# Kernel optimization log

Measured on AMD Instinct MI355X. Metric: run time of the kernel, lower is better.

## Reference

```python
import jax, jax.numpy as jnp
import numpy as np

N_MELS = 128
N_STATE = 1024
N_HEAD = 8
N_LAYER = 6
STRIDE = 2
HEAD_DIM = N_STATE // N_HEAD  # 128; must equal N_MELS for the rope buffer to broadcast
B = 8
T = 4096


def setup_inputs():
    key = jax.random.key(0)
    ks = iter(jax.random.split(key, 40))
    def rn(shape, s=0.02):
        return jax.random.normal(next(ks), shape, dtype=jnp.float32) * s
    L, D, F = N_LAYER, N_STATE, 4 * N_STATE
    inp = {}
    inp['x'] = jax.random.normal(next(ks), (B, N_MELS, T), dtype=jnp.float32)
    inp['x_len'] = jax.random.randint(next(ks), (B,), T // 2, T + 1)
    inp['conv1_w'] = rn((D, N_MELS, 3))
    inp['conv1_b'] = jnp.zeros((D,), jnp.float32)
    inp['conv2_w'] = rn((D, D, 3))
    inp['conv2_b'] = jnp.zeros((D,), jnp.float32)
    inp['attn_ln_w'] = jnp.ones((L, D), jnp.float32)
    inp['attn_ln_b'] = jnp.zeros((L, D), jnp.float32)
    inp['q_w'] = rn((L, D, D)); inp['q_b'] = jnp.zeros((L, D), jnp.float32)
    inp['k_w'] = rn((L, D, D))
    inp['v_w'] = rn((L, D, D)); inp['v_b'] = jnp.zeros((L, D), jnp.float32)
    inp['out_w'] = rn((L, D, D)); inp['out_b'] = jnp.zeros((L, D), jnp.float32)
    inp['mlp_ln_w'] = jnp.ones((L, D), jnp.float32)
    inp['mlp_ln_b'] = jnp.zeros((L, D), jnp.float32)
    inp['mlp1_w'] = rn((L, F, D)); inp['mlp1_b'] = jnp.zeros((L, F), jnp.float32)
    inp['mlp2_w'] = rn((L, D, F)); inp['mlp2_b'] = jnp.zeros((L, D), jnp.float32)
    return inp


def _ln(x, w, b, eps=1e-5):
    x = x.astype(jnp.float32)
    m = jnp.mean(x, -1, keepdims=True)
    v = jnp.mean((x - m) ** 2, -1, keepdims=True)
    return (x - m) * jax.lax.rsqrt(v + eps) * w + b


def _conv1d(x, w, b, stride):
    # x: [B, Cin, T]; w: [Cout, Cin, K] (torch OIH layout); pad=1
    y = jax.lax.conv_general_dilated(x, w, (stride,), [(1, 1)],
                                     dimension_numbers=('NCH', 'OIH', 'NCH'))
    return y + b[None, :, None]


def reference(x, x_len, conv1_w, conv1_b, conv2_w, conv2_b,
              attn_ln_w, attn_ln_b, q_w, q_b, k_w, v_w, v_b, out_w, out_b,
              mlp_ln_w, mlp_ln_b, mlp1_w, mlp1_b, mlp2_w, mlp2_b):
    Tin = x.shape[-1]
    h = jax.nn.gelu(_conv1d(x, conv1_w, conv1_b, STRIDE), approximate=False)
    h = jax.nn.gelu(_conv1d(h, conv2_w, conv2_b, 2), approximate=False)
    h = jnp.transpose(h, (0, 2, 1))  # [B, S, D]
    S = h.shape[1]

    # non-pad mask over original mel frames, subsampled like the conv stack
    mask = jnp.arange(Tin)[None, :] < x_len[:, None]
    mask = mask[:, (Tin + 1) % 2::2]
    if STRIDE == 2:
        Tm = mask.shape[-1]
        mask = mask[:, (Tm + 1) % 2::2]
    bias = ((1.0 - mask.astype(jnp.float32)) * -1.0e10)[:, None, None, :]  # [B,1,1,S]

    # rotary embedding table (freqs_cis as cos/sin), dim == HEAD_DIM == N_MELS
    half = HEAD_DIM // 2
    freqs = 1.0 / (10000.0 ** (jnp.arange(0, HEAD_DIM, 2, dtype=jnp.float32) / HEAD_DIM))
    ang = jnp.arange(S, dtype=jnp.float32)[:, None] * freqs[None, :]  # [S, half]
    cos = jnp.cos(ang)[None, :, None, :]
    sin = jnp.sin(ang)[None, :, None, :]
    scale = HEAD_DIM ** (-0.25)

    def rot(t):  # t: [B,S,H,HEAD_DIM], interleaved (re, im) pairs
        tr = t.reshape(t.shape[0], t.shape[1], N_HEAD, half, 2)
        re, im = tr[..., 0], tr[..., 1]
        return jnp.stack([re * cos - im * sin, re * sin + im * cos], -1)\
                  .reshape(t.shape[0], t.shape[1], N_HEAD, HEAD_DIM)

    def block(carry, p):
        aw, ab, qw, qb, kw, vw, vb, ow, ob, mw, mb, w1, b1, w2, b2 = p
        y = _ln(carry, aw, ab)
        q = y @ qw.T + qb
        k = y @ kw.T          # key has no bias
        v = y @ vw.T + vb
        Bb, Ss = q.shape[0], q.shape[1]
        q = rot(q.reshape(Bb, Ss, N_HEAD, HEAD_DIM)) * scale
        k = rot(k.reshape(Bb, Ss, N_HEAD, HEAD_DIM)) * scale
        v = v.reshape(Bb, Ss, N_HEAD, HEAD_DIM)
        qk = jnp.einsum('bqhd,bkhd->bhqk', q, k) + bias
        w = jax.nn.softmax(qk.astype(jnp.float32), axis=-1)
        o = jnp.einsum('bhqk,bkhd->bqhd', w, v).reshape(Bb, Ss, N_STATE)
        carry = carry + o @ ow.T + ob
        y = _ln(carry, mw, mb)
        y = jax.nn.gelu(y @ w1.T + b1, approximate=False) @ w2.T + b2
        return carry + y, None

    params = (attn_ln_w, attn_ln_b, q_w, q_b, k_w, v_w, v_b, out_w, out_b,
              mlp_ln_w, mlp_ln_b, mlp1_w, mlp1_b, mlp2_w, mlp2_b)
    h, _ = jax.lax.scan(block, h, params)

    y_len = (x_len + 1) // 2
    if STRIDE == 2:
        y_len = (y_len + 1) // 2
    return h, y_len
```

## Files before the change

kernel.cpp:

```cpp
#include <hip/hip_runtime.h>
#include <hip/hip_bf16.h>
#include <cstdint>
#include <cstddef>


typedef __bf16 bf16_t;
typedef __bf16 bf16x8 __attribute__((ext_vector_type(8)));
typedef __bf16 bf16x4 __attribute__((ext_vector_type(4)));
typedef float  floatx4 __attribute__((ext_vector_type(4)));

#define NB   8
#define NS   1024
#define ND   1024
#define NT   4096
#define NT1  2048

#define MFMA16(a, b, c) __builtin_amdgcn_mfma_f32_16x16x32_bf16(a, b, c, 0, 0, 0)

#define SBAR() do { __builtin_amdgcn_sched_barrier(0); \
                    __builtin_amdgcn_s_barrier();      \
                    __builtin_amdgcn_sched_barrier(0); } while (0)

__device__ __forceinline__ float gelu_f(float x) {
  const float t = 1.5957691216057308f * (x + 0.044715f * x * x * x);
  return x / (1.0f + __expf(-t));
}

__device__ __forceinline__ void gload16(const void* g, void* l) {
  __builtin_amdgcn_global_load_lds(
      (__attribute__((address_space(1))) void*)(const_cast<void*>(g)),
      (__attribute__((address_space(3))) void*)l, 16, 0, 0);
}

enum { EPI_BF16 = 0, EPI_GELU_BF16 = 2, EPI_GELU_F32 = 3, EPI_RES_F32 = 4, EPI_QKV = 5 };

template<int EPI>
__global__ __launch_bounds__(512)
void gemm_bt(const bf16_t* __restrict__ A, long lda,
             const bf16_t* __restrict__ Bm, long ldb,
             void* Cv, long ldc,
             const float* __restrict__ bias, const float* res,
             int K, int swz,
             bf16_t* out2, bf16_t* out3, const float* __restrict__ bias2,
             const float2* __restrict__ rtab)
{
  __shared__ bf16_t sA[3][4096];
  __shared__ bf16_t sB[3][4096];
  const int tid  = threadIdx.x;
  const int wid  = tid >> 6;
  const int lane = tid & 63;
  const int lo = lane & 15, g = lane >> 4;
  const int wr = wid >> 2, wc = wid & 3;

  int bx = blockIdx.x, by = blockIdx.y;
  if (swz) {
    const int gx = gridDim.x;
    const int n  = gx * gridDim.y;
    int id = bx + by * gx;
    id = (id & 7) * (n >> 3) + (id >> 3);
    bx = id % gx; by = id / gx;
  }
  const int m0 = bx * 128, n0 = by * 128;
  const int NTK = K >> 5;

  const int lrow = lane >> 2;
  const int lcol = 8 * ((lane & 3) ^ ((lane >> 3) & 3));

  auto stage = [&](int t) {
    if (t >= NTK) return;
    const int kb = t << 5;
    bf16_t* dA = &sA[t % 3][0];
    bf16_t* dB = &sB[t % 3][0];
    const int seg = wid;
    gload16(A  + (long)(m0 + seg * 16 + lrow) * lda + kb + lcol, dA + seg * 512);
    gload16(Bm + (long)(n0 + seg * 16 + lrow) * ldb + kb + lcol, dB + seg * 512);
  };

  const int rslot = 16 * (g ^ ((lo >> 1) & 3));

  floatx4 acc[4][2] = {};

  stage(0); stage(1);
  asm volatile("s_waitcnt vmcnt(2)" ::: "memory");
  SBAR();

#pragma unroll 1
  for (int s = 0; s < NTK; ++s) {
    stage(s + 2);
    const bf16_t* bufA = &sA[s % 3][0];
    const bf16_t* bufB = &sB[s % 3][0];
    bf16x8 av[4], bv[2];
#pragma unroll
    for (int i = 0; i < 4; ++i)
      av[i] = *(const bf16x8*)((const char*)(bufA + (wr * 64 + i * 16 + lo) * 32) + rslot);
#pragma unroll
    for (int i = 0; i < 2; ++i)
      bv[i] = *(const bf16x8*)((const char*)(bufB + (wc * 32 + i * 16 + lo) * 32) + rslot);
#pragma unroll
    for (int mi = 0; mi < 4; ++mi)
#pragma unroll
      for (int ni = 0; ni < 2; ++ni)
        acc[mi][ni] = MFMA16(av[mi], bv[ni], acc[mi][ni]);
    if (s + 2 < NTK) { asm volatile("s_waitcnt vmcnt(2)" ::: "memory"); }
    else             { asm volatile("s_waitcnt vmcnt(0)" ::: "memory"); }
    SBAR();
  }

  if constexpr (EPI == EPI_QKV) {
    const int sect = n0 >> 10;
#pragma unroll
    for (int ni = 0; ni < 2; ++ni) {
      const int col = n0 + wc * 32 + ni * 16 + lo;
      const int c10 = col & 1023;
      float bvs = 0.0f;
      if (sect == 0) bvs = bias[c10];
      else if (sect == 2) bvs = bias2[c10];
#pragma unroll
      for (int mi = 0; mi < 4; ++mi) {
#pragma unroll
        for (int r = 0; r < 4; ++r) {
          const int row = m0 + wr * 64 + mi * 16 + g * 4 + r;
          const int s = row & 1023;
          float val = acc[mi][ni][r] + bvs;
          if (sect < 2) {
            const float2 t = rtab[(s << 6) + ((col & 127) >> 1)];
            const float p = __shfl_xor(val, 1);
            val = val * t.x + p * ((col & 1) ? t.y : -t.y);
            bf16_t* dst = sect ? out2 : (bf16_t*)Cv;
            dst[(long)row * 1024 + c10] = (bf16_t)val;
          } else {
            out3[((long)(row >> 10) << 20) + ((long)(col - 2048) << 10) + s] = (bf16_t)val;
          }
        }
      }
    }
    return;
  }

#pragma unroll
  for (int ni = 0; ni < 2; ++ni) {
    const int col = n0 + wc * 32 + ni * 16 + lo;
    const float bvs = bias ? bias[col] : 0.0f;
#pragma unroll
    for (int mi = 0; mi < 4; ++mi) {
#pragma unroll
      for (int r = 0; r < 4; ++r) {
        const int row = m0 + wr * 64 + mi * 16 + g * 4 + r;
        float v = acc[mi][ni][r] + bvs;
        if constexpr (EPI == EPI_BF16) {
          ((bf16_t*)Cv)[(long)row * ldc + col] = (bf16_t)v;
        } else if constexpr (EPI == EPI_GELU_BF16) {
          ((bf16_t*)Cv)[(long)row * ldc + col] = (bf16_t)gelu_f(v);
        } else if constexpr (EPI == EPI_GELU_F32) {
          ((float*)Cv)[(long)row * ldc + col] = gelu_f(v);
        } else {
          const long idx = (long)row * ldc + col;
          ((float*)Cv)[idx] = res[idx] + v;
        }
      }
    }
  }
}

__global__ __launch_bounds__(256)
void flash_kernel(const bf16_t* __restrict__ q, const bf16_t* __restrict__ k,
                  const bf16_t* __restrict__ vt, bf16_t* __restrict__ o,
                  const int* __restrict__ xlen)
{
  __shared__ bf16_t sK[2][4096];
  __shared__ bf16_t sV[2][4096];
  __shared__ bf16_t sP[4][2048];
  const int tid = threadIdx.x, w = tid >> 6, lane = tid & 63;
  const int lo = lane & 15, g = lane >> 4;
  const int bh = blockIdx.y, b = bh >> 3, h = bh & 7;
  const int q0 = blockIdx.x * 128 + w * 32;
  const int nv  = xlen[b] >> 2;
  const int nkt = (nv + 63) >> 6;
  const long base = (long)b * 1048576 + (long)h * 128;
  const bf16_t* Qp = q + base;
  const bf16_t* Kp = k + base;
  const bf16_t* Vp = vt + (long)b * 1048576 + ((long)h << 17);

  auto stageKV = [&](int kt, int buf) {
    const int kv0 = kt << 6;
#pragma unroll
    for (int j = 0; j < 4; ++j) {
      const int seg = (w << 2) + j;
      {
        const int row = (seg << 2) + (lane >> 4);
        const int col = ((lane & 15) << 3) ^ ((row & 7) << 3);
        gload16(Kp + (long)(kv0 + row) * 1024 + col, &sK[buf][seg * 512]);
      }
      {
        const int row = (seg << 3) + (lane >> 3);
        const int col = ((lane & 7) << 3) ^ ((row & 7) << 3);
        gload16(Vp + (long)row * 1024 + kv0 + col, &sV[buf][seg * 512]);
      }
    }
  };

  bf16x8 qf[2][4];
#pragma unroll
  for (int mi = 0; mi < 2; ++mi)
#pragma unroll
    for (int ks = 0; ks < 4; ++ks)
      qf[mi][ks] = *reinterpret_cast<const bf16x8*>(
          Qp + (long)(q0 + mi * 16 + lo) * 1024 + ks * 32 + g * 8);

  floatx4 of[2][8] = {};
  float m[2][4], l[2][4];
#pragma unroll
  for (int mi = 0; mi < 2; ++mi)
#pragma unroll
    for (int r = 0; r < 4; ++r) { m[mi][r] = -1e30f; l[mi][r] = 0.0f; }

  const char* kbase = (const char*)&sK[0][0];
  const char* vbase = (const char*)&sV[0][0];
  char* pbase = (char*)&sP[w][0];
  const int swzL = (lo & 7) << 4;

  stageKV(0, 0);
  __syncthreads();
  int cur = 0;
#pragma unroll 1
  for (int kt = 0; kt < nkt; ++kt) {
    const int kv0 = kt << 6;
    if (kt + 1 < nkt) stageKV(kt + 1, cur ^ 1);

    floatx4 s[2][4] = {};
#pragma unroll
    for (int ni = 0; ni < 4; ++ni) {
#pragma unroll
      for (int ks = 0; ks < 4; ++ks) {
        const bf16x8 bv = *reinterpret_cast<const bf16x8*>(
            kbase + cur * 8192 + (ni * 16 + lo) * 256 + ((ks * 64 + (g << 4)) ^ swzL));
        s[0][ni] = MFMA16(qf[0][ks], bv, s[0][ni]);
        s[1][ni] = MFMA16(qf[1][ks], bv, s[1][ni]);
      }
    }

#pragma unroll
    for (int mi = 0; mi < 2; ++mi) {
#pragma unroll
      for (int r = 0; r < 4; ++r) {
        float vv[4]; float pm = -1e30f;
#pragma unroll
        for (int ni = 0; ni < 4; ++ni) {
          float val = s[mi][ni][r];
          if (kv0 + ni * 16 + lo >= nv) val = -1e30f;
          vv[ni] = val; pm = fmaxf(pm, val);
        }
        pm = fmaxf(pm, __shfl_xor(pm, 1)); pm = fmaxf(pm, __shfl_xor(pm, 2));
        pm = fmaxf(pm, __shfl_xor(pm, 4)); pm = fmaxf(pm, __shfl_xor(pm, 8));
        const float mo = m[mi][r];
        const float mn = fmaxf(mo, pm);
        const float sc = __expf(mo - mn);
        const int qrow = mi * 16 + g * 4 + r;
        const int sw = (qrow & 7) << 4;
        float ss = 0.0f;
#pragma unroll
        for (int ni = 0; ni < 4; ++ni) {
          const float p = __expf(vv[ni] - mn);
          ss += p;
          *(bf16_t*)(pbase + qrow * 128 + (((ni << 5) + (lo << 1)) ^ sw)) = (bf16_t)p;
        }
        ss += __shfl_xor(ss, 1); ss += __shfl_xor(ss, 2);
        ss += __shfl_xor(ss, 4); ss += __shfl_xor(ss, 8);
        l[mi][r] = l[mi][r] * sc + ss;
        m[mi][r] = mn;
#pragma unroll
        for (int nd = 0; nd < 8; ++nd) of[mi][nd][r] *= sc;
      }
    }

    asm volatile("s_waitcnt lgkmcnt(0)" ::: "memory");
    __builtin_amdgcn_sched_barrier(0);

#pragma unroll
    for (int ks = 0; ks < 2; ++ks) {
      bf16x8 av0 = *reinterpret_cast<const bf16x8*>(
          pbase + (0 * 16 + lo) * 128 + (((ks << 6) + (g << 4)) ^ swzL));
      bf16x8 av1 = *reinterpret_cast<const bf16x8*>(
          pbase + (1 * 16 + lo) * 128 + (((ks << 6) + (g << 4)) ^ swzL));
#pragma unroll
      for (int nd = 0; nd < 8; ++nd) {
        const bf16x8 bv = *reinterpret_cast<const bf16x8*>(
            vbase + cur * 8192 + (nd * 16 + lo) * 128 + (((ks << 6) + (g << 4)) ^ swzL));
        of[0][nd] = MFMA16(av0, bv, of[0][nd]);
        of[1][nd] = MFMA16(av1, bv, of[1][nd]);
      }
    }
    __syncthreads();
    cur ^= 1;
  }

#pragma unroll
  for (int mi = 0; mi < 2; ++mi)
#pragma unroll
    for (int r = 0; r < 4; ++r) {
      const float inv = 1.0f / l[mi][r];
      const long rb = base + (long)(q0 + mi * 16 + g * 4 + r) * 1024;
#pragma unroll
      for (int nd = 0; nd < 8; ++nd)
        o[rb + nd * 16 + lo] = (bf16_t)(of[mi][nd][r] * inv);
    }
}

__global__ __launch_bounds__(256)
void ln_kernel(const float* __restrict__ x, bf16_t* __restrict__ y,
               const float* __restrict__ w, const float* __restrict__ b)
{
  const long row = blockIdx.x;
  const float4 v = reinterpret_cast<const float4*>(x + row * ND)[threadIdx.x];
  float s  = v.x + v.y + v.z + v.w;
  float ss = v.x * v.x + v.y * v.y + v.z * v.z + v.w * v.w;
#pragma unroll
  for (int off = 32; off; off >>= 1) { s += __shfl_down(s, off); ss += __shfl_down(ss, off); }
  __shared__ float sh[8];
  if ((threadIdx.x & 63) == 0) { sh[threadIdx.x >> 6] = s; sh[4 + (threadIdx.x >> 6)] = ss; }
  __syncthreads();
  const float tot  = sh[0] + sh[1] + sh[2] + sh[3];
  const float tot2 = sh[4] + sh[5] + sh[6] + sh[7];
  const float mean = tot * (1.0f / ND);
  const float var  = tot2 * (1.0f / ND) - mean * mean;
  const float rstd = rsqrtf(var + 1e-5f);
  const int i0 = threadIdx.x * 4;
  const float vv[4] = {v.x, v.y, v.z, v.w};
  bf16x4 o;
#pragma unroll
  for (int j = 0; j < 4; ++j)
    o[j] = (bf16_t)((vv[j] - mean) * rstd * w[i0 + j] + b[i0 + j]);
  reinterpret_cast<bf16x4*>(y + row * ND)[threadIdx.x] = o;
}

__global__ __launch_bounds__(256)
void rtab_kernel(float2* __restrict__ tab)
{
  const int idx = blockIdx.x * 256 + threadIdx.x;
  const int s = idx >> 6, i = idx & 63;
  const float freq = __expf((float)i * -0.14391156831212787f);
  float sn, cs;
  sincosf((float)s * freq, &sn, &cs);
  const float sc = 0.29730177875068026f;
  tab[idx] = make_float2(cs * sc, sn * sc);
}

__global__ __launch_bounds__(256)
void im2col1_kernel(const float* __restrict__ x, bf16_t* __restrict__ a)
{
  const long idx = (long)blockIdx.x * 256 + threadIdx.x;
  if (idx >= (long)NB * NT1 * 384) return;
  const int  k = (int)(idx % 384);
  const long m = idx / 384;
  const int i = k / 3, kk = k - 3 * i;
  const int t = (int)(m & (NT1 - 1));
  const int b = (int)(m >> 11);
  const int tt = 2 * t + kk - 1;
  float v = 0.0f;
  if (tt >= 0 && tt < NT) v = x[((long)b * 128 + i) * NT + tt];
  a[idx] = (bf16_t)v;
}

__global__ __launch_bounds__(256)
void im2col2_kernel(const bf16_t* __restrict__ h1, bf16_t* __restrict__ a)
{
  const long idx = (long)blockIdx.x * 256 + threadIdx.x;
  if (idx >= (long)NB * NS * 3072) return;
  const int  k = (int)(idx % 3072);
  const long m = idx / 3072;
  const int i = k / 3, kk = k - 3 * i;
  const int t = (int)(m & (NS - 1));
  const int b = (int)(m >> 10);
  const int tt = 2 * t + kk - 1;
  bf16_t v = (bf16_t)0.0f;
  if (tt >= 0 && tt < NT1) v = h1[((long)b * NT1 + tt) * ND + i];
  a[idx] = v;
}

__global__ void ylen_kernel(const int* __restrict__ xlen, float* __restrict__ ylen)
{
  const int b = threadIdx.x;
  if (b < NB) {
    const int y1 = (xlen[b] + 1) >> 1;
    ylen[b] = (float)((y1 + 1) >> 1);
  }
}

__global__ __launch_bounds__(256)
void cvt_kernel(const float* __restrict__ in, bf16_t* __restrict__ out, long n)
{
  const long i = ((long)blockIdx.x * 256 + threadIdx.x) * 4;
  if (i >= n) return;
  const float4 v = *reinterpret_cast<const float4*>(in + i);
  bf16x4 o;
  o[0] = (bf16_t)v.x; o[1] = (bf16_t)v.y; o[2] = (bf16_t)v.z; o[3] = (bf16_t)v.w;
  *reinterpret_cast<bf16x4*>(out + i) = o;
}

__global__ __launch_bounds__(256)
void cvt3_kernel(const float* __restrict__ a, const float* __restrict__ b,
                 const float* __restrict__ c, bf16_t* __restrict__ out)
{
  const long i = ((long)blockIdx.x * 256 + threadIdx.x) * 4;
  const float* src; long j;
  if (i < 1048576)      { src = a; j = i; }
  else if (i < 2097152) { src = b; j = i - 1048576; }
  else                  { src = c; j = i - 2097152; }
  const float4 v = *reinterpret_cast<const float4*>(src + j);
  bf16x4 o;
  o[0] = (bf16_t)v.x; o[1] = (bf16_t)v.y; o[2] = (bf16_t)v.z; o[3] = (bf16_t)v.w;
  *reinterpret_cast<bf16x4*>(out + i) = o;
}

__global__ __launch_bounds__(256)
void cvt2_kernel(const float* __restrict__ a, const float* __restrict__ b,
                 bf16_t* __restrict__ out)
{
  const long i = ((long)blockIdx.x * 256 + threadIdx.x) * 4;
  const float* src; long j;
  if (i < 4194304) { src = a; j = i; }
  else             { src = b; j = i - 4194304; }
  const float4 v = *reinterpret_cast<const float4*>(src + j);
  bf16x4 o;
  o[0] = (bf16_t)v.x; o[1] = (bf16_t)v.y; o[2] = (bf16_t)v.z; o[3] = (bf16_t)v.w;
  *reinterpret_cast<bf16x4*>(out + i) = o;
}

extern "C" void kernel_launch(void* const* d_in, const int* in_sizes, int n_in,
                              void* d_out, int out_size, void* d_ws, size_t ws_size,
                              hipStream_t stream)
{
  const float* x         = (const float*)d_in[0];
  const int*   x_len     = (const int*)  d_in[1];
  const float* conv1_w   = (const float*)d_in[2];
  const float* conv1_b   = (const float*)d_in[3];
  const float* conv2_w   = (const float*)d_in[4];
  const float* conv2_b   = (const float*)d_in[5];
  const float* attn_ln_w = (const float*)d_in[6];
  const float* attn_ln_b = (const float*)d_in[7];
  const float* q_w   = (const float*)d_in[8];
  const float* q_b   = (const float*)d_in[9];
  const float* k_w   = (const float*)d_in[10];
  const float* v_w   = (const float*)d_in[11];
  const float* v_b   = (const float*)d_in[12];
  const float* out_w = (const float*)d_in[13];
  const float* out_b = (const float*)d_in[14];
  const float* mlp_ln_w = (const float*)d_in[15];
  const float* mlp_ln_b = (const float*)d_in[16];
  const float* mlp1_w = (const float*)d_in[17];
  const float* mlp1_b = (const float*)d_in[18];
  const float* mlp2_w = (const float*)d_in[19];
  const float* mlp2_b = (const float*)d_in[20];
  float* outp = (float*)d_out;
  (void)in_sizes; (void)n_in; (void)out_size;

  const long MB = 1024L * 1024;
  char* ws = (char*)d_ws;
  size_t off = 0;
  auto alloc = [&](size_t bytes) -> char* {
    char* p = ws + off;
    off += (bytes + 255) & ~(size_t)255;
    return p;
  };
  bf16_t* ybuf  = (bf16_t*)alloc(16 * MB);
  bf16_t* qbuf  = (bf16_t*)alloc(16 * MB);
  char*   R     = alloc(64 * MB);
  char*   wA    = alloc(24 * MB);
  const size_t required = off;

  bf16_t* a1  = ybuf;
  bf16_t* h1  = qbuf;
  bf16_t* a2  = (bf16_t*)(R + 16 * MB);
  bf16_t* c2w = (bf16_t*)wA;
  bf16_t* c1w = (bf16_t*)(wA + 8 * MB);
  float2* rtab = (float2*)(wA + 6 * MB);
  bf16_t* wqkv = (bf16_t*)wA;
  bf16_t* vt   = (bf16_t*)(wA + 8 * MB);
  bf16_t* wo   = (bf16_t*)(wA + 16 * MB);
  bf16_t* w1b  = (bf16_t*)(wA + 8 * MB);
  bf16_t* w2b  = (bf16_t*)(wA + 16 * MB);
  bf16_t* kbuf = (bf16_t*)R;
  bf16_t* hid  = (bf16_t*)R;

  if (required > ws_size) {
    ylen_kernel<<<dim3(1), 64, 0, stream>>>(x_len, outp + 8L * 1024 * 1024);
    return;
  }

  auto cvt = [&](const float* in, bf16_t* o, long n) {
    cvt_kernel<<<dim3((unsigned)(n / 1024)), 256, 0, stream>>>(in, o, n);
  };

  rtab_kernel<<<dim3(256), 256, 0, stream>>>(rtab);

  cvt(conv1_w, c1w, 1024L * 384);
  cvt(conv2_w, c2w, 1024L * 3072);
  im2col1_kernel<<<dim3((unsigned)((16384L * 384) / 256)), 256, 0, stream>>>(x, a1);
  gemm_bt<EPI_GELU_BF16><<<dim3(128, 8), 512, 0, stream>>>(
      a1, 384, c1w, 384, h1, 1024, conv1_b, nullptr, 384, 1,
      nullptr, nullptr, nullptr, nullptr);
  im2col2_kernel<<<dim3((unsigned)((8192L * 3072) / 256)), 256, 0, stream>>>(h1, a2);
  gemm_bt<EPI_GELU_F32><<<dim3(64, 8), 512, 0, stream>>>(
      a2, 3072, c2w, 3072, outp , 1024, conv2_b, nullptr, 3072, 1,
      nullptr, nullptr, nullptr, nullptr);

  float* carry = outp;

  for (int l = 0; l < 6; ++l) {
    cvt3_kernel<<<dim3(3072), 256, 0, stream>>>(
        q_w + (long)l * 1048576, k_w + (long)l * 1048576, v_w + (long)l * 1048576, wqkv);

    ln_kernel<<<dim3(8192), 256, 0, stream>>>(carry, ybuf, attn_ln_w + l * 1024, attn_ln_b + l * 1024);

    gemm_bt<EPI_QKV><<<dim3(64, 24), 512, 0, stream>>>(
        ybuf, 1024, wqkv, 1024, qbuf, 1024,
        q_b + l * 1024, nullptr, 1024, 1, kbuf, vt, v_b + l * 1024, rtab);

    flash_kernel<<<dim3(8, 64), 256, 0, stream>>>(qbuf, kbuf, vt, qbuf, x_len);

    cvt(out_w + (long)l * 1048576, wo, 1048576);
    gemm_bt<EPI_RES_F32><<<dim3(64, 8), 512, 0, stream>>>(
        qbuf, 1024, wo, 1024, carry, 1024,
        out_b + l * 1024, carry, 1024, 1, nullptr, nullptr, nullptr, nullptr);

    cvt2_kernel<<<dim3(8192), 256, 0, stream>>>(
        mlp1_w + (long)l * 4194304, mlp2_w + (long)l * 4194304, w1b);

    ln_kernel<<<dim3(8192), 256, 0, stream>>>(carry, ybuf, mlp_ln_w + l * 1024, mlp_ln_b + l * 1024);

    gemm_bt<EPI_GELU_BF16><<<dim3(64, 32), 512, 0, stream>>>(
        ybuf, 1024, w1b, 1024, hid, 4096,
        mlp1_b + (long)l * 4096, nullptr, 1024, 1, nullptr, nullptr, nullptr, nullptr);
    gemm_bt<EPI_RES_F32><<<dim3(64, 8), 512, 0, stream>>>(
        hid, 4096, w2b, 4096, carry, 1024,
        mlp2_b + l * 1024, carry, 4096, 1, nullptr, nullptr, nullptr, nullptr);
  }

  ylen_kernel<<<dim3(1), 64, 0, stream>>>(x_len, outp + 8L * 1024 * 1024);
}
```

Before: 3.010 ms.

## Shrink flash tiles, add lazy rescale and priority hints, merge per-layer weight casts

The flash attention kernel now gives each wave 16 query rows and processes 32-key tiles. It doubles the grid to 1024 blocks and remaps block indices so all heads of a query tile run adjacently, with a launch bound of 4 blocks per CU. It skips the online-softmax rescale when the running max grows by at most 8, and raises wave priority around the MFMA sections. The separate per-layer weight conversion kernels are merged into one launch, with workspace buffers relaid to fit. The smaller tiles mean more loop iterations and barriers per key, and the lazy rescale lets unnormalized exponentials grow larger.

```diff
diff --git a/kernel.cpp b/kernel.cpp
--- a/kernel.cpp
+++ b/kernel.cpp
@@ -162,148 +162,155 @@
   }
 }
 
-__global__ __launch_bounds__(256)
+__global__ __launch_bounds__(256, 4)
 void flash_kernel(const bf16_t* __restrict__ q, const bf16_t* __restrict__ k,
                   const bf16_t* __restrict__ vt, bf16_t* __restrict__ o,
                   const int* __restrict__ xlen)
 {
   __shared__ bf16_t sK[2][4096];
   __shared__ bf16_t sV[2][4096];
-  __shared__ bf16_t sP[4][2048];
+  __shared__ bf16_t sP[4][512];
   const int tid = threadIdx.x, w = tid >> 6, lane = tid & 63;
   const int lo = lane & 15, g = lane >> 4;
-  const int bh = blockIdx.y, b = bh >> 3, h = bh & 7;
-  const int q0 = blockIdx.x * 128 + w * 32;
+  const int hid = blockIdx.x + (blockIdx.y << 4);
+  const int h   = hid & 7;
+  const int qx  = (hid >> 3) & 15;
+  const int b   = hid >> 7;
+  const int q0 = qx * 64 + w * 16;
   const int nv  = xlen[b] >> 2;
-  const int nkt = (nv + 63) >> 6;
+  const int nkt = (nv + 31) >> 5;
   const long base = (long)b * 1048576 + (long)h * 128;
   const bf16_t* Qp = q + base;
   const bf16_t* Kp = k + base;
   const bf16_t* Vp = vt + (long)b * 1048576 + ((long)h << 17);
 
   auto stageKV = [&](int kt, int buf) {
-    const int kv0 = kt << 6;
-#pragma unroll
-    for (int j = 0; j < 4; ++j) {
-      const int seg = (w << 2) + j;
+    const int kv0 = kt << 5;
+#pragma unroll
+    for (int jj = 0; jj < 2; ++jj) {
+      const int seg = (w << 1) + jj;
       {
         const int row = (seg << 2) + (lane >> 4);
         const int col = ((lane & 15) << 3) ^ ((row & 7) << 3);
         gload16(Kp + (long)(kv0 + row) * 1024 + col, &sK[buf][seg * 512]);
       }
       {
-        const int row = (seg << 3) + (lane >> 3);
-        const int col = ((lane & 7) << 3) ^ ((row & 7) << 3);
+        const int row = (seg << 4) + (lane >> 2);
+        const int col = ((lane & 3) << 3) ^ ((row & 3) << 3);
         gload16(Vp + (long)row * 1024 + kv0 + col, &sV[buf][seg * 512]);
       }
     }
   };
 
-  bf16x8 qf[2][4];
-#pragma unroll
-  for (int mi = 0; mi < 2; ++mi)
-#pragma unroll
-    for (int ks = 0; ks < 4; ++ks)
-      qf[mi][ks] = *reinterpret_cast<const bf16x8*>(
-          Qp + (long)(q0 + mi * 16 + lo) * 1024 + ks * 32 + g * 8);
-
-  floatx4 of[2][8] = {};
-  float m[2][4], l[2][4];
-#pragma unroll
-  for (int mi = 0; mi < 2; ++mi)
-#pragma unroll
-    for (int r = 0; r < 4; ++r) { m[mi][r] = -1e30f; l[mi][r] = 0.0f; }
+  bf16x8 qf[4];
+#pragma unroll
+  for (int ks = 0; ks < 4; ++ks)
+    qf[ks] = *reinterpret_cast<const bf16x8*>(
+        Qp + (long)(q0 + lo) * 1024 + ks * 32 + g * 8);
+
+  floatx4 of[8] = {};
+  float m[4], l[4];
+#pragma unroll
+  for (int r = 0; r < 4; ++r) { m[r] = -1e30f; l[r] = 0.0f; }
 
   const char* kbase = (const char*)&sK[0][0];
   const char* vbase = (const char*)&sV[0][0];
   char* pbase = (char*)&sP[w][0];
-  const int swzL = (lo & 7) << 4;
+  const int swzK = (lo & 7) << 4;
+  const int swzV = (lo & 3) << 4;
 
   stageKV(0, 0);
   __syncthreads();
   int cur = 0;
 #pragma unroll 1
   for (int kt = 0; kt < nkt; ++kt) {
-    const int kv0 = kt << 6;
+    const int kv0 = kt << 5;
     if (kt + 1 < nkt) stageKV(kt + 1, cur ^ 1);
 
-    floatx4 s[2][4] = {};
-#pragma unroll
-    for (int ni = 0; ni < 4; ++ni) {
+    floatx4 s[2] = {};
+    __builtin_amdgcn_s_setprio(1);
+#pragma unroll
+    for (int ni = 0; ni < 2; ++ni) {
 #pragma unroll
       for (int ks = 0; ks < 4; ++ks) {
         const bf16x8 bv = *reinterpret_cast<const bf16x8*>(
-            kbase + cur * 8192 + (ni * 16 + lo) * 256 + ((ks * 64 + (g << 4)) ^ swzL));
-        s[0][ni] = MFMA16(qf[0][ks], bv, s[0][ni]);
-        s[1][ni] = MFMA16(qf[1][ks], bv, s[1][ni]);
-      }
-    }
-
-#pragma unroll
-    for (int mi = 0; mi < 2; ++mi) {
-#pragma unroll
-      for (int r = 0; r < 4; ++r) {
-        float vv[4]; float pm = -1e30f;
-#pragma unroll
-        for (int ni = 0; ni < 4; ++ni) {
-          float val = s[mi][ni][r];
-          if (kv0 + ni * 16 + lo >= nv) val = -1e30f;
-          vv[ni] = val; pm = fmaxf(pm, val);
-        }
-        pm = fmaxf(pm, __shfl_xor(pm, 1)); pm = fmaxf(pm, __shfl_xor(pm, 2));
-        pm = fmaxf(pm, __shfl_xor(pm, 4)); pm = fmaxf(pm, __shfl_xor(pm, 8));
-        const float mo = m[mi][r];
-        const float mn = fmaxf(mo, pm);
-        const float sc = __expf(mo - mn);
-        const int qrow = mi * 16 + g * 4 + r;
-        const int sw = (qrow & 7) << 4;
-        float ss = 0.0f;
-#pragma unroll
-        for (int ni = 0; ni < 4; ++ni) {
-          const float p = __expf(vv[ni] - mn);
-          ss += p;
-          *(bf16_t*)(pbase + qrow * 128 + (((ni << 5) + (lo << 1)) ^ sw)) = (bf16_t)p;
-        }
-        ss += __shfl_xor(ss, 1); ss += __shfl_xor(ss, 2);
-        ss += __shfl_xor(ss, 4); ss += __shfl_xor(ss, 8);
-        l[mi][r] = l[mi][r] * sc + ss;
-        m[mi][r] = mn;
-#pragma unroll
-        for (int nd = 0; nd < 8; ++nd) of[mi][nd][r] *= sc;
-      }
+            kbase + cur * 8192 + (ni * 16 + lo) * 256 + ((ks * 64 + (g << 4)) ^ swzK));
+        s[ni] = MFMA16(qf[ks], bv, s[ni]);
+      }
+    }
+    __builtin_amdgcn_s_setprio(0);
+
+    float pmv[4];
+#pragma unroll
+    for (int r = 0; r < 4; ++r) {
+      float pm = -1e30f;
+#pragma unroll
+      for (int ni = 0; ni < 2; ++ni) {
+        float val = s[ni][r];
+        if (kv0 + ni * 16 + lo >= nv) val = -1e30f;
+        pm = fmaxf(pm, val);
+      }
+      pm = fmaxf(pm, __shfl_xor(pm, 1)); pm = fmaxf(pm, __shfl_xor(pm, 2));
+      pm = fmaxf(pm, __shfl_xor(pm, 4)); pm = fmaxf(pm, __shfl_xor(pm, 8));
+      pmv[r] = pm;
+    }
+    const bool skip = __all((pmv[0] <= m[0] + 8.0f) & (pmv[1] <= m[1] + 8.0f) &
+                            (pmv[2] <= m[2] + 8.0f) & (pmv[3] <= m[3] + 8.0f));
+
+#pragma unroll
+    for (int r = 0; r < 4; ++r) {
+      float mn = m[r];
+      if (!skip) {
+        mn = fmaxf(m[r], pmv[r]);
+        const float sc = __expf(m[r] - mn);
+        l[r] *= sc;
+#pragma unroll
+        for (int nd = 0; nd < 8; ++nd) of[nd][r] *= sc;
+        m[r] = mn;
+      }
+      const int qrow = g * 4 + r;
+      const int sw = (qrow & 3) << 4;
+      float ss = 0.0f;
+#pragma unroll
+      for (int ni = 0; ni < 2; ++ni) {
+        float val = s[ni][r];
+        if (kv0 + ni * 16 + lo >= nv) val = -1e30f;
+        const float p = __expf(val - mn);
+        ss += p;
+        *(bf16_t*)(pbase + qrow * 64 + (((ni << 5) + (lo << 1)) ^ sw)) = (bf16_t)p;
+      }
+      ss += __shfl_xor(ss, 1); ss += __shfl_xor(ss, 2);
+      ss += __shfl_xor(ss, 4); ss += __shfl_xor(ss, 8);
+      l[r] += ss;
     }
 
     asm volatile("s_waitcnt lgkmcnt(0)" ::: "memory");
     __builtin_amdgcn_sched_barrier(0);
 
-#pragma unroll
-    for (int ks = 0; ks < 2; ++ks) {
-      bf16x8 av0 = *reinterpret_cast<const bf16x8*>(
-          pbase + (0 * 16 + lo) * 128 + (((ks << 6) + (g << 4)) ^ swzL));
-      bf16x8 av1 = *reinterpret_cast<const bf16x8*>(
-          pbase + (1 * 16 + lo) * 128 + (((ks << 6) + (g << 4)) ^ swzL));
+    __builtin_amdgcn_s_setprio(1);
+    {
+      const bf16x8 av = *reinterpret_cast<const bf16x8*>(
+          pbase + lo * 64 + ((g << 4) ^ swzV));
 #pragma unroll
       for (int nd = 0; nd < 8; ++nd) {
         const bf16x8 bv = *reinterpret_cast<const bf16x8*>(
-            vbase + cur * 8192 + (nd * 16 + lo) * 128 + (((ks << 6) + (g << 4)) ^ swzL));
-        of[0][nd] = MFMA16(av0, bv, of[0][nd]);
-        of[1][nd] = MFMA16(av1, bv, of[1][nd]);
-      }
-    }
+            vbase + cur * 8192 + (nd * 16 + lo) * 64 + ((g << 4) ^ swzV));
+        of[nd] = MFMA16(av, bv, of[nd]);
+      }
+    }
+    __builtin_amdgcn_s_setprio(0);
     __syncthreads();
     cur ^= 1;
   }
 
 #pragma unroll
-  for (int mi = 0; mi < 2; ++mi)
-#pragma unroll
-    for (int r = 0; r < 4; ++r) {
-      const float inv = 1.0f / l[mi][r];
-      const long rb = base + (long)(q0 + mi * 16 + g * 4 + r) * 1024;
-#pragma unroll
-      for (int nd = 0; nd < 8; ++nd)
-        o[rb + nd * 16 + lo] = (bf16_t)(of[mi][nd][r] * inv);
-    }
+  for (int r = 0; r < 4; ++r) {
+    const float inv = 1.0f / l[r];
+    const long rb = base + (long)(q0 + g * 4 + r) * 1024;
+#pragma unroll
+    for (int nd = 0; nd < 8; ++nd)
+      o[rb + nd * 16 + lo] = (bf16_t)(of[nd][r] * inv);
+  }
 }
 
 __global__ __launch_bounds__(256)
@@ -398,32 +405,26 @@
 }
 
 __global__ __launch_bounds__(256)
-void cvt3_kernel(const float* __restrict__ a, const float* __restrict__ b,
-                 const float* __restrict__ c, bf16_t* __restrict__ out)
+void cvt_layer_kernel(const float* __restrict__ qw, const float* __restrict__ kw,
+                      const float* __restrict__ vw, const float* __restrict__ ow,
+                      const float* __restrict__ w1, const float* __restrict__ w2,
+                      bf16_t* __restrict__ wqkv, bf16_t* __restrict__ wo,
+                      bf16_t* __restrict__ w1b, bf16_t* __restrict__ w2b)
 {
   const long i = ((long)blockIdx.x * 256 + threadIdx.x) * 4;
-  const float* src; long j;
-  if (i < 1048576)      { src = a; j = i; }
-  else if (i < 2097152) { src = b; j = i - 1048576; }
-  else                  { src = c; j = i - 2097152; }
-  const float4 v = *reinterpret_cast<const float4*>(src + j);
+  const float* src; bf16_t* dst;
+  if (i < 3145728) {
+    dst = wqkv + i;
+    if (i < 1048576)      { src = qw + i; }
+    else if (i < 2097152) { src = kw + (i - 1048576); }
+    else                  { src = vw + (i - 2097152); }
+  } else if (i < 4194304) { src = ow + (i - 3145728); dst = wo  + (i - 3145728); }
+  else if (i < 8388608)   { src = w1 + (i - 4194304); dst = w1b + (i - 4194304); }
+  else                    { src = w2 + (i - 8388608); dst = w2b + (i - 8388608); }
+  const float4 v = *reinterpret_cast<const float4*>(src);
   bf16x4 o;
   o[0] = (bf16_t)v.x; o[1] = (bf16_t)v.y; o[2] = (bf16_t)v.z; o[3] = (bf16_t)v.w;
-  *reinterpret_cast<bf16x4*>(out + i) = o;
-}
-
-__global__ __launch_bounds__(256)
-void cvt2_kernel(const float* __restrict__ a, const float* __restrict__ b,
-                 bf16_t* __restrict__ out)
-{
-  const long i = ((long)blockIdx.x * 256 + threadIdx.x) * 4;
-  const float* src; long j;
-  if (i < 4194304) { src = a; j = i; }
-  else             { src = b; j = i - 4194304; }
-  const float4 v = *reinterpret_cast<const float4*>(src + j);
-  bf16x4 o;
-  o[0] = (bf16_t)v.x; o[1] = (bf16_t)v.y; o[2] = (bf16_t)v.z; o[3] = (bf16_t)v.w;
-  *reinterpret_cast<bf16x4*>(out + i) = o;
+  *reinterpret_cast<bf16x4*>(dst) = o;
 }
 
 extern "C" void kernel_launch(void* const* d_in, const int* in_sizes, int n_in,
@@ -465,7 +466,7 @@
   bf16_t* ybuf  = (bf16_t*)alloc(16 * MB);
   bf16_t* qbuf  = (bf16_t*)alloc(16 * MB);
   char*   R     = alloc(64 * MB);
-  char*   wA    = alloc(24 * MB);
+  char*   wA    = alloc(25 * MB);
   const size_t required = off;
 
   bf16_t* a1  = ybuf;
@@ -475,11 +476,11 @@
   bf16_t* c1w = (bf16_t*)(wA + 8 * MB);
   float2* rtab = (float2*)(wA + 6 * MB);
   bf16_t* wqkv = (bf16_t*)wA;
-  bf16_t* vt   = (bf16_t*)(wA + 8 * MB);
-  bf16_t* wo   = (bf16_t*)(wA + 16 * MB);
-  bf16_t* w1b  = (bf16_t*)(wA + 8 * MB);
-  bf16_t* w2b  = (bf16_t*)(wA + 16 * MB);
+  bf16_t* wo   = (bf16_t*)(wA + 6 * MB + 512 * 1024);
+  bf16_t* w1b  = (bf16_t*)(wA + 9 * MB);
+  bf16_t* w2b  = (bf16_t*)(wA + 17 * MB);
   bf16_t* kbuf = (bf16_t*)R;
+  bf16_t* vt   = (bf16_t*)(R + 16 * MB);
   bf16_t* hid  = (bf16_t*)R;
 
   if (required > ws_size) {
@@ -507,8 +508,10 @@
   float* carry = outp;
 
   for (int l = 0; l < 6; ++l) {
-    cvt3_kernel<<<dim3(3072), 256, 0, stream>>>(
-        q_w + (long)l * 1048576, k_w + (long)l * 1048576, v_w + (long)l * 1048576, wqkv);
+    cvt_layer_kernel<<<dim3(12288), 256, 0, stream>>>(
+        q_w + (long)l * 1048576, k_w + (long)l * 1048576, v_w + (long)l * 1048576,
+        out_w + (long)l * 1048576, mlp1_w + (long)l * 4194304, mlp2_w + (long)l * 4194304,
+        wqkv, wo, w1b, w2b);
 
     ln_kernel<<<dim3(8192), 256, 0, stream>>>(carry, ybuf, attn_ln_w + l * 1024, attn_ln_b + l * 1024);
 
@@ -516,15 +519,11 @@
         ybuf, 1024, wqkv, 1024, qbuf, 1024,
         q_b + l * 1024, nullptr, 1024, 1, kbuf, vt, v_b + l * 1024, rtab);
 
-    flash_kernel<<<dim3(8, 64), 256, 0, stream>>>(qbuf, kbuf, vt, qbuf, x_len);
-
-    cvt(out_w + (long)l * 1048576, wo, 1048576);
+    flash_kernel<<<dim3(16, 64), 256, 0, stream>>>(qbuf, kbuf, vt, qbuf, x_len);
+
     gemm_bt<EPI_RES_F32><<<dim3(64, 8), 512, 0, stream>>>(
         qbuf, 1024, wo, 1024, carry, 1024,
         out_b + l * 1024, carry, 1024, 1, nullptr, nullptr, nullptr, nullptr);
-
-    cvt2_kernel<<<dim3(8192), 256, 0, stream>>>(
-        mlp1_w + (long)l * 4194304, mlp2_w + (long)l * 4194304, w1b);
 
     ln_kernel<<<dim3(8192), 256, 0, stream>>>(carry, ybuf, mlp_ln_w + l * 1024, mlp_ln_b + l * 1024);
 
```

Result: no change. 2.959 ms (-1.7%).
